# Kernel optimization log

Measured on AMD Instinct MI355X. Metric: run time of the kernel, lower is better.

Reference implementation:

```python
import jax, jax.numpy as jnp
import numpy as np

# 3x3 window hardcoded in the original forward (symmetric, so corr == conv)
_WINDOW = np.array([[0.09474166, 0.11831801, 0.09474166],
                    [0.11831801, 0.14776132, 0.11831801],
                    [0.09474166, 0.11831801, 0.09474166]], dtype=np.float32)


def _filt(img, kern):
    # img: [B,1,H,W], kern: [1,1,3,3]; SAME padding (cv2 border effects are
    # confined to a 1-px rim, which the [5:-5,5:-5] crop removes anyway)
    return jax.lax.conv_general_dilated(
        img, kern, window_strides=(1, 1), padding='SAME',
        dimension_numbers=('NCHW', 'OIHW', 'NCHW'))


def setup_inputs() -> dict:
    key = jax.random.key(0)
    k1, k2 = jax.random.split(key)
    B, C, H, W = 64, 1, 512, 512
    X = jax.random.uniform(k1, (B, C, H, W), dtype=jnp.float32)
    Y = jax.random.uniform(k2, (B, C, H, W), dtype=jnp.float32)
    return {"X": X, "Y": Y}


def reference(X, Y):
    kern = jnp.asarray(_WINDOW)[None, None]  # [1,1,3,3]
    crop = lambda t: t[:, 0, 5:-5, 5:-5]      # channel 0, crop 5-px border

    mu1 = crop(_filt(X, kern))
    mu2 = crop(_filt(Y, kern))
    sigma1_sq = crop(_filt(X * X, kern)) - mu1 * mu1
    sigma2_sq = crop(_filt(Y * Y, kern)) - mu2 * mu2
    sigma12 = crop(_filt(X * Y, kern)) - mu1 * mu2

    # per-sample loss = mean over cropped HW; batch_loss = sum over samples
    loss = sigma1_sq * sigma2_sq - 2.0 * sigma12  # [B, H-10, W-10]
    return jnp.sum(jnp.mean(loss, axis=(1, 2)))
```

## Files before the change

### kernel.cpp

```cpp
#include <hip/hip_runtime.h>

#define A_W 0.30780133f
#define B_W 0.38439735f

#define IMG_W 512
#define CROP_LO 5
#define CROP_HI 507
#define STRIP 16
#define NSTRIPS 32
#define BT 256

struct H10 { float a1[2], a2[2], a11[2], a22[2], a12[2]; };

__device__ __forceinline__ void hsum(const float4& x, const float4& y, H10& h) {
    float xx0 = x.x * x.x, xx1 = x.y * x.y, xx2 = x.z * x.z, xx3 = x.w * x.w;
    float yy0 = y.x * y.x, yy1 = y.y * y.y, yy2 = y.z * y.z, yy3 = y.w * y.w;
    float xy0 = x.x * y.x, xy1 = x.y * y.y, xy2 = x.z * y.z, xy3 = x.w * y.w;
    h.a1[0]  = A_W * (x.x + x.z) + B_W * x.y;
    h.a1[1]  = A_W * (x.y + x.w) + B_W * x.z;
    h.a2[0]  = A_W * (y.x + y.z) + B_W * y.y;
    h.a2[1]  = A_W * (y.y + y.w) + B_W * y.z;
    h.a11[0] = A_W * (xx0 + xx2) + B_W * xx1;
    h.a11[1] = A_W * (xx1 + xx3) + B_W * xx2;
    h.a22[0] = A_W * (yy0 + yy2) + B_W * yy1;
    h.a22[1] = A_W * (yy1 + yy3) + B_W * yy2;
    h.a12[0] = A_W * (xy0 + xy2) + B_W * xy1;
    h.a12[1] = A_W * (xy1 + xy3) + B_W * xy2;
}

#define GLOAD(dst, ptr) \
    asm volatile("global_load_dwordx4 %0, %1, off" : "=v"(dst) : "v"(ptr))
#define WAITCNT(N)                                              \
    asm volatile("s_waitcnt vmcnt(" #N ")" ::: "memory");       \
    __builtin_amdgcn_sched_barrier(0)

__global__ __launch_bounds__(BT, 4) void ssim_loss_main(
    const float* __restrict__ X, const float* __restrict__ Y,
    float* __restrict__ partials) {
    const int t  = threadIdx.x;
    const int c0 = 4 + 2 * t;
    const int lc = min(c0, 508) - 1;
    const int b  = blockIdx.y;
    const int r0 = CROP_LO + STRIP * blockIdx.x;

    const float* Xb = X + (size_t)b * IMG_W * IMG_W;
    const float* Yb = Y + (size_t)b * IMG_W * IMG_W;

    const float cm0 = (c0     >= CROP_LO && c0     < CROP_HI) ? 1.0f : 0.0f;
    const float cm1 = (c0 + 1 >= CROP_LO && c0 + 1 < CROP_HI) ? 1.0f : 0.0f;

    auto adrX = [&](int row) { return Xb + (size_t)min(row, IMG_W - 1) * IMG_W + lc; };
    auto adrY = [&](int row) { return Yb + (size_t)min(row, IMG_W - 1) * IMG_W + lc; };

    float4 px0, py0, px1, py1;
    GLOAD(px0, adrX(r0 - 1)); GLOAD(py0, adrY(r0 - 1));
    GLOAD(px1, adrX(r0));     GLOAD(py1, adrY(r0));

    float4 bx[2][4], by[2][4];
#pragma unroll
    for (int rr = 0; rr < 4; ++rr) {
        GLOAD(bx[0][rr], adrX(r0 + 1 + rr));
        GLOAD(by[0][rr], adrY(r0 + 1 + rr));
    }
    WAITCNT(8);

    H10 P, C, N;
    hsum(px0, py0, P);
    hsum(px1, py1, C);

    float acc = 0.0f;
#pragma unroll
    for (int g = 0; g < 4; ++g) {
        if (g < 3) {
#pragma unroll
            for (int rr = 0; rr < 4; ++rr) {
                GLOAD(bx[(g + 1) & 1][rr], adrX(r0 + 4 * g + 5 + rr));
                GLOAD(by[(g + 1) & 1][rr], adrY(r0 + 4 * g + 5 + rr));
            }
            WAITCNT(8);
        } else {
            WAITCNT(0);
        }
#pragma unroll
        for (int rr = 0; rr < 4; ++rr) {
            hsum(bx[g & 1][rr], by[g & 1][rr], N);
            float racc = 0.0f;
#pragma unroll
            for (int k = 0; k < 2; ++k) {
                float s1  = A_W * (P.a1[k]  + N.a1[k])  + B_W * C.a1[k];
                float s2  = A_W * (P.a2[k]  + N.a2[k])  + B_W * C.a2[k];
                float s11 = A_W * (P.a11[k] + N.a11[k]) + B_W * C.a11[k];
                float s22 = A_W * (P.a22[k] + N.a22[k]) + B_W * C.a22[k];
                float s12 = A_W * (P.a12[k] + N.a12[k]) + B_W * C.a12[k];
                float v1 = s11 - s1 * s1;
                float v2 = s22 - s2 * s2;
                float cv = s12 - s1 * s2;
                racc += (k ? cm1 : cm0) * (v1 * v2 - 2.0f * cv);
            }
            acc += (r0 + 4 * g + rr < CROP_HI) ? racc : 0.0f;
            P = C; C = N;
        }
    }

    for (int off = 32; off > 0; off >>= 1) acc += __shfl_down(acc, off, 64);
    __shared__ float wsum[BT / 64];
    if ((t & 63) == 0) wsum[t >> 6] = acc;
    __syncthreads();
    if (t == 0)
        partials[blockIdx.x + NSTRIPS * b] = wsum[0] + wsum[1] + wsum[2] + wsum[3];
}

__global__ __launch_bounds__(256) void ssim_loss_finalize(
    const float* __restrict__ partials, int n, float* __restrict__ out) {
    const int tid = threadIdx.x;
    float s = 0.0f;
    for (int i = tid; i < n; i += 256) s += partials[i];
    for (int off = 32; off > 0; off >>= 1) s += __shfl_down(s, off, 64);
    __shared__ float wsum[4];
    if ((tid & 63) == 0) wsum[tid >> 6] = s;
    __syncthreads();
    if (tid == 0) {
        float total = wsum[0] + wsum[1] + wsum[2] + wsum[3];
        out[0] = total * (1.0f / 252004.0f);
    }
}

extern "C" void kernel_launch(void* const* d_in, const int* in_sizes, int n_in,
                              void* d_out, int out_size, void* d_ws, size_t ws_size,
                              hipStream_t stream) {
    const float* X = (const float*)d_in[0];
    const float* Y = (const float*)d_in[1];
    float* out = (float*)d_out;
    float* partials = (float*)d_ws;

    dim3 grid(NSTRIPS, 64);
    ssim_loss_main<<<grid, BT, 0, stream>>>(X, Y, partials);
    ssim_loss_finalize<<<1, 256, 0, stream>>>(partials, NSTRIPS * 64, out);
}
```

Baseline: 30.30 us.

## Fuse finalize into main kernel via last-block atomic and double strip height

Removes the separate finalize kernel launch: each block writes its partial, bumps an atomic counter, and the last block to finish reduces all partials and writes the output. Strips grow from 16 to 32 rows, halving the grid and the halo reloads per block, and the prefetch group shrinks from 4 to 2 rows per stage. A hipMemsetAsync is added to reset the counter, which itself costs a stream operation, and the smaller grid (1024 blocks) can reduce latency hiding on the GPU.

```diff
diff --git a/kernel.cpp b/kernel.cpp
--- a/kernel.cpp
+++ b/kernel.cpp
@@ -6,9 +6,10 @@
 #define IMG_W 512
 #define CROP_LO 5
 #define CROP_HI 507
-#define STRIP 16
-#define NSTRIPS 32
+#define STRIP 32
+#define NSTRIPS 16
 #define BT 256
+#define NBLK (NSTRIPS * 64)
 
 struct H10 { float a1[2], a2[2], a11[2], a22[2], a12[2]; };
 
@@ -36,12 +37,14 @@
 
 __global__ __launch_bounds__(BT, 4) void ssim_loss_main(
     const float* __restrict__ X, const float* __restrict__ Y,
-    float* __restrict__ partials) {
+    float* __restrict__ partials, unsigned int* __restrict__ counter,
+    float* __restrict__ out) {
     const int t  = threadIdx.x;
     const int c0 = 4 + 2 * t;
     const int lc = min(c0, 508) - 1;
     const int b  = blockIdx.y;
     const int r0 = CROP_LO + STRIP * blockIdx.x;
+    const int bid = blockIdx.x + NSTRIPS * b;
 
     const float* Xb = X + (size_t)b * IMG_W * IMG_W;
     const float* Yb = Y + (size_t)b * IMG_W * IMG_W;
@@ -56,13 +59,13 @@
     GLOAD(px0, adrX(r0 - 1)); GLOAD(py0, adrY(r0 - 1));
     GLOAD(px1, adrX(r0));     GLOAD(py1, adrY(r0));
 
-    float4 bx[2][4], by[2][4];
+    float4 bx[2][2], by[2][2];
 #pragma unroll
-    for (int rr = 0; rr < 4; ++rr) {
+    for (int rr = 0; rr < 2; ++rr) {
         GLOAD(bx[0][rr], adrX(r0 + 1 + rr));
         GLOAD(by[0][rr], adrY(r0 + 1 + rr));
     }
-    WAITCNT(8);
+    WAITCNT(4);
 
     H10 P, C, N;
     hsum(px0, py0, P);
@@ -70,19 +73,19 @@
 
     float acc = 0.0f;
 #pragma unroll
-    for (int g = 0; g < 4; ++g) {
-        if (g < 3) {
+    for (int g = 0; g < 16; ++g) {
+        if (g < 15) {
 #pragma unroll
-            for (int rr = 0; rr < 4; ++rr) {
-                GLOAD(bx[(g + 1) & 1][rr], adrX(r0 + 4 * g + 5 + rr));
-                GLOAD(by[(g + 1) & 1][rr], adrY(r0 + 4 * g + 5 + rr));
+            for (int rr = 0; rr < 2; ++rr) {
+                GLOAD(bx[(g + 1) & 1][rr], adrX(r0 + 2 * g + 3 + rr));
+                GLOAD(by[(g + 1) & 1][rr], adrY(r0 + 2 * g + 3 + rr));
             }
-            WAITCNT(8);
+            WAITCNT(4);
         } else {
             WAITCNT(0);
         }
 #pragma unroll
-        for (int rr = 0; rr < 4; ++rr) {
+        for (int rr = 0; rr < 2; ++rr) {
             hsum(bx[g & 1][rr], by[g & 1][rr], N);
             float racc = 0.0f;
 #pragma unroll
@@ -97,31 +100,34 @@
                 float cv = s12 - s1 * s2;
                 racc += (k ? cm1 : cm0) * (v1 * v2 - 2.0f * cv);
             }
-            acc += (r0 + 4 * g + rr < CROP_HI) ? racc : 0.0f;
+            acc += (r0 + 2 * g + rr < CROP_HI) ? racc : 0.0f;
             P = C; C = N;
         }
     }
 
     for (int off = 32; off > 0; off >>= 1) acc += __shfl_down(acc, off, 64);
     __shared__ float wsum[BT / 64];
+    __shared__ int amLast;
     if ((t & 63) == 0) wsum[t >> 6] = acc;
     __syncthreads();
-    if (t == 0)
-        partials[blockIdx.x + NSTRIPS * b] = wsum[0] + wsum[1] + wsum[2] + wsum[3];
-}
+    if (t == 0) {
+        partials[bid] = wsum[0] + wsum[1] + wsum[2] + wsum[3];
+        __threadfence();
+        unsigned int old = atomicAdd(counter, 1u);
+        amLast = (old == NBLK - 1) ? 1 : 0;
+    }
+    __syncthreads();
 
-__global__ __launch_bounds__(256) void ssim_loss_finalize(
-    const float* __restrict__ partials, int n, float* __restrict__ out) {
-    const int tid = threadIdx.x;
-    float s = 0.0f;
-    for (int i = tid; i < n; i += 256) s += partials[i];
-    for (int off = 32; off > 0; off >>= 1) s += __shfl_down(s, off, 64);
-    __shared__ float wsum[4];
-    if ((tid & 63) == 0) wsum[tid >> 6] = s;
-    __syncthreads();
-    if (tid == 0) {
-        float total = wsum[0] + wsum[1] + wsum[2] + wsum[3];
-        out[0] = total * (1.0f / 252004.0f);
+    if (amLast) {
+        __threadfence();
+        float s = 0.0f;
+#pragma unroll
+        for (int i = 0; i < NBLK / BT; ++i) s += partials[t + BT * i];
+        for (int off = 32; off > 0; off >>= 1) s += __shfl_down(s, off, 64);
+        if ((t & 63) == 0) wsum[t >> 6] = s;
+        __syncthreads();
+        if (t == 0)
+            out[0] = (wsum[0] + wsum[1] + wsum[2] + wsum[3]) * (1.0f / 252004.0f);
     }
 }
 
@@ -131,9 +137,10 @@
     const float* X = (const float*)d_in[0];
     const float* Y = (const float*)d_in[1];
     float* out = (float*)d_out;
-    float* partials = (float*)d_ws;
+    unsigned int* counter = (unsigned int*)d_ws;
+    float* partials = (float*)((char*)d_ws + 256);
 
+    hipMemsetAsync(d_ws, 0, 4, stream);
     dim3 grid(NSTRIPS, 64);
-    ssim_loss_main<<<grid, BT, 0, stream>>>(X, Y, partials);
-    ssim_loss_finalize<<<1, 256, 0, stream>>>(partials, NSTRIPS * 64, out);
+    ssim_loss_main<<<grid, BT, 0, stream>>>(X, Y, partials, counter, out);
 }
```

Result: slower. 61.60 us (+103.3%).
